# Performance work log

Hardware: AMD Instinct MI355X
Metric: run time of the kernel (lower is better)

The kernel has to match this reference:

```python
import jax, jax.numpy as jnp
import numpy as np

B, N, F_IN, D = 32768, 4, 512, 64  # N fixed to 4 by the max_pool(4,1)+reshape


def setup_inputs() -> dict:
    key = jax.random.key(0)
    k1, k2, k3, k4 = jax.random.split(key, 4)
    scale = 1.0 / np.sqrt(F_IN)
    return {
        "drug": jax.random.normal(k1, (B, N, F_IN), dtype=jnp.float32),
        "Wk": jax.random.normal(k2, (F_IN, D), dtype=jnp.float32) * scale,
        "Wq": jax.random.normal(k3, (F_IN, D), dtype=jnp.float32) * scale,
        "Wv": jax.random.normal(k4, (F_IN, D), dtype=jnp.float32) * scale,
    }


def reference(drug, Wk, Wq, Wv):
    # projections: torch nn.Linear(bias=False) -> x @ W  (W stored as [in, out] here)
    k = jnp.einsum("bnf,fd->bnd", drug, Wk)
    q = jnp.einsum("bnf,fd->bnd", drug, Wq)
    v = jnp.einsum("bnf,fd->bnd", drug, Wv)
    # score = bmm(K, Q^T); NOTE: no 1/sqrt(d) scaling, matching the source
    score = jnp.einsum("bnd,bmd->bnm", k, q)  # [B, N, N]
    attn = jax.nn.softmax(score, axis=2)
    out = jnp.einsum("bnm,bmd->bnd", attn, v)  # [B, N, D]
    # max_pool2d kernel (4,1), stride (4,1) over N=4 -> max over axis 1, then reshape [B, D]
    return jnp.max(out, axis=1)
```

## Files before the change

kernel.cpp:

```cpp
#include <hip/hip_runtime.h>
#include <hip/hip_fp16.h>

#define BTOT   32768
#define FIN    512
#define KSTEPS 16
#define NTILES 12
#define WH_ELEMS (KSTEPS * NTILES * 64 * 8)
#define CHUNK_HALVES (NTILES * 64 * 8)
#define KQ_HALVES (KSTEPS * 8 * 512)
#define KQ_BYTES  (KQ_HALVES * 2)
#define WAVES  8
#define ROWTILES 4
#define ROWS_PER_BLOCK (WAVES * 16 * ROWTILES)
#define NBLOCKS (BTOT * 4 / ROWS_PER_BLOCK)

using half8   = __attribute__((ext_vector_type(8))) _Float16;
using floatx4 = __attribute__((ext_vector_type(4))) float;

#define GLOAD_LDS16(gp, lp)                                                  \
    __builtin_amdgcn_global_load_lds(                                        \
        (const __attribute__((address_space(1))) void*)(gp),                 \
        (__attribute__((address_space(3))) void*)(lp), 16, 0, 0)

__global__ void convert_w_kernel(const float* __restrict__ Wk,
                                 const float* __restrict__ Wq,
                                 const float* __restrict__ Wv,
                                 _Float16* __restrict__ Wh) {
    int idx = blockIdx.x * blockDim.x + threadIdx.x;
    if (idx >= WH_ELEMS) return;
    int j    = idx & 7;
    int lane = (idx >> 3) & 63;
    int t    = (idx >> 9) % NTILES;
    int kk   = idx / CHUNK_HALVES;
    int k = kk * 32 + (lane >> 4) * 8 + j;
    int n = t * 16 + (lane & 15);
    const float* src = (n < 64) ? Wk : (n < 128) ? Wq : Wv;
    _Float16 val = (_Float16)src[k * 64 + (n & 63)];
    size_t dst = (t < 8)
        ? ((size_t)(kk * 8 + t) * 512 + lane * 8 + j)
        : (size_t)KQ_HALVES + ((size_t)(kk * 4 + (t - 8)) * 512 + lane * 8 + j);
    Wh[dst] = val;
}

__global__ __launch_bounds__(512, 2) void attn_fused_kernel(
        const float* __restrict__ drug,
        const _Float16* __restrict__ Wh,
        float* __restrict__ out)
{
    extern __shared__ __align__(16) char lds[];

    const int tid  = threadIdx.x;
    const int wave = tid >> 6;
    const int lane = tid & 63;
    const int quad = lane >> 4;
    const int l15  = lane & 15;

    {
        const char* gk = (const char*)Wh;
#pragma unroll
        for (int i = 0; i < 16; ++i) {
            const int off = i * 8192 + wave * 1024;
            GLOAD_LDS16(gk + off + lane * 16, lds + off);
        }
    }

    const half8* vf = (const half8*)(Wh + KQ_HALVES) + lane;

    const int rowbase = blockIdx.x * ROWS_PER_BLOCK + wave * 16 + l15;
    const float* arow = drug + (size_t)rowbase * FIN + quad * 8;
    float4 a0 = ((const float4*)arow)[0];
    float4 a1 = ((const float4*)arow)[1];
    half8 v0 = vf[0], v1 = vf[64], v2 = vf[128], v3 = vf[192];

    asm volatile("s_waitcnt vmcnt(0)" ::: "memory");
    __builtin_amdgcn_s_barrier();

    const int bbase = blockIdx.x * (ROWS_PER_BLOCK / 4) + wave * 4 + quad;

#pragma unroll 1
    for (int rt = 0; rt < ROWTILES; ++rt) {
        floatx4 acc[NTILES];
#pragma unroll
        for (int t = 0; t < NTILES; ++t) acc[t] = (floatx4){0.f, 0.f, 0.f, 0.f};

        const float* pfrow = (rt < ROWTILES - 1) ? arow + 128 * FIN : arow;

#pragma unroll 1
        for (int k = 0; k < KSTEPS; ++k) {
            float4 n0, n1;
            half8 w0, w1, w2, w3;
            {
                const float4* ap = (k < KSTEPS - 1)
                    ? (const float4*)(arow + (k + 1) * 32)
                    : (const float4*)pfrow;
                n0 = ap[0];
                n1 = ap[1];
                const half8* vp = (k < KSTEPS - 1) ? vf + (k + 1) * 256 : vf;
                w0 = vp[0]; w1 = vp[64]; w2 = vp[128]; w3 = vp[192];
            }

            half8 af;
            af[0] = (_Float16)a0.x; af[1] = (_Float16)a0.y;
            af[2] = (_Float16)a0.z; af[3] = (_Float16)a0.w;
            af[4] = (_Float16)a1.x; af[5] = (_Float16)a1.y;
            af[6] = (_Float16)a1.z; af[7] = (_Float16)a1.w;

            const _Float16* lh = (const _Float16*)(lds + k * 8192);
#pragma unroll
            for (int t = 0; t < 8; ++t) {
                half8 bf = *((const half8*)(lh + t * 512 + lane * 8));
                acc[t] = __builtin_amdgcn_mfma_f32_16x16x32_f16(af, bf, acc[t], 0, 0, 0);
            }
            acc[8]  = __builtin_amdgcn_mfma_f32_16x16x32_f16(af, v0, acc[8],  0, 0, 0);
            acc[9]  = __builtin_amdgcn_mfma_f32_16x16x32_f16(af, v1, acc[9],  0, 0, 0);
            acc[10] = __builtin_amdgcn_mfma_f32_16x16x32_f16(af, v2, acc[10], 0, 0, 0);
            acc[11] = __builtin_amdgcn_mfma_f32_16x16x32_f16(af, v3, acc[11], 0, 0, 0);

            a0 = n0; a1 = n1;
            v0 = w0; v1 = w1; v2 = w2; v3 = w3;
        }
        arow += 128 * FIN;

        float p[4][4];
#pragma unroll
        for (int n = 0; n < 4; ++n)
#pragma unroll
            for (int m = 0; m < 4; ++m) {
                float s = 0.f;
#pragma unroll
                for (int t = 0; t < 4; ++t) s += acc[t][n] * acc[4 + t][m];
                p[n][m] = s;
            }

#pragma unroll
        for (int mask = 1; mask < 16; mask <<= 1) {
#pragma unroll
            for (int n = 0; n < 4; ++n)
#pragma unroll
                for (int m = 0; m < 4; ++m)
                    p[n][m] += __shfl_xor(p[n][m], mask, 64);
        }

        float res[4] = {-INFINITY, -INFINITY, -INFINITY, -INFINITY};
#pragma unroll
        for (int n = 0; n < 4; ++n) {
            float mx = fmaxf(fmaxf(p[n][0], p[n][1]), fmaxf(p[n][2], p[n][3]));
            float e0 = __expf(p[n][0] - mx);
            float e1 = __expf(p[n][1] - mx);
            float e2 = __expf(p[n][2] - mx);
            float e3 = __expf(p[n][3] - mx);
            float inv = 1.f / (e0 + e1 + e2 + e3);
#pragma unroll
            for (int t = 0; t < 4; ++t) {
                float o = (e0 * acc[8 + t][0] + e1 * acc[8 + t][1] +
                           e2 * acc[8 + t][2] + e3 * acc[8 + t][3]) * inv;
                res[t] = fmaxf(res[t], o);
            }
        }

        const int b = bbase + rt * 32;
#pragma unroll
        for (int t = 0; t < 4; ++t)
            out[b * 64 + t * 16 + l15] = res[t];
    }
}

extern "C" void kernel_launch(void* const* d_in, const int* in_sizes, int n_in,
                              void* d_out, int out_size, void* d_ws, size_t ws_size,
                              hipStream_t stream) {
    const float* drug = (const float*)d_in[0];
    const float* Wk   = (const float*)d_in[1];
    const float* Wq   = (const float*)d_in[2];
    const float* Wv   = (const float*)d_in[3];
    float* out = (float*)d_out;
    _Float16* Wh = (_Float16*)d_ws;

    static bool attr_set = false;
    if (!attr_set) {
        hipFuncSetAttribute((const void*)attn_fused_kernel,
                            hipFuncAttributeMaxDynamicSharedMemorySize, KQ_BYTES);
        attr_set = true;
    }

    convert_w_kernel<<<(WH_ELEMS + 255) / 256, 256, 0, stream>>>(Wk, Wq, Wv, Wh);
    attn_fused_kernel<<<NBLOCKS, 512, KQ_BYTES, stream>>>(drug, Wh, out);
}
```

Measured before the change: 371.7 us.

## Process two row tiles per k-step and stage half of Wv in LDS

The main loop now keeps two 16-row A fragments and two accumulator sets, so each K/Q/V B-fragment loaded from LDS or registers feeds two MFMAs. Two of the four V tiles now sit in LDS (160KB total) instead of being reloaded from global memory every k-step. The row loop becomes two passes of paired tiles, with a shared epilogue helper. The aim is to halve LDS and global weight traffic per MFMA. The cost is doubled accumulator and prefetch register pressure under launch_bounds(512,2), which risks spilling, and a larger LDS footprint that limits blocks per CU.

```diff
diff --git a/kernel.cpp b/kernel.cpp
--- a/kernel.cpp
+++ b/kernel.cpp
@@ -6,12 +6,11 @@
 #define KSTEPS 16
 #define NTILES 12
 #define WH_ELEMS (KSTEPS * NTILES * 64 * 8)
-#define CHUNK_HALVES (NTILES * 64 * 8)
-#define KQ_HALVES (KSTEPS * 8 * 512)
-#define KQ_BYTES  (KQ_HALVES * 2)
+#define KQ_HALVES  65536
+#define V23_BASE   81920
+#define LDS_BYTES  163840
 #define WAVES  8
-#define ROWTILES 4
-#define ROWS_PER_BLOCK (WAVES * 16 * ROWTILES)
+#define ROWS_PER_BLOCK 512
 #define NBLOCKS (BTOT * 4 / ROWS_PER_BLOCK)
 
 using half8   = __attribute__((ext_vector_type(8))) _Float16;
@@ -31,15 +30,61 @@
     int j    = idx & 7;
     int lane = (idx >> 3) & 63;
     int t    = (idx >> 9) % NTILES;
-    int kk   = idx / CHUNK_HALVES;
+    int kk   = idx / (NTILES * 64 * 8);
     int k = kk * 32 + (lane >> 4) * 8 + j;
     int n = t * 16 + (lane & 15);
     const float* src = (n < 64) ? Wk : (n < 128) ? Wq : Wv;
     _Float16 val = (_Float16)src[k * 64 + (n & 63)];
-    size_t dst = (t < 8)
-        ? ((size_t)(kk * 8 + t) * 512 + lane * 8 + j)
-        : (size_t)KQ_HALVES + ((size_t)(kk * 4 + (t - 8)) * 512 + lane * 8 + j);
+    size_t dst;
+    if (t < 8)
+        dst = (size_t)(kk * 8 + t) * 512 + lane * 8 + j;
+    else if (t < 10)
+        dst = (size_t)KQ_HALVES + (size_t)(kk * 2 + (t - 8)) * 512 + lane * 8 + j;
+    else
+        dst = (size_t)V23_BASE + (size_t)(kk * 2 + (t - 10)) * 512 + lane * 8 + j;
     Wh[dst] = val;
+}
+
+__device__ __forceinline__ void attn_epilogue(const floatx4 (&acc)[NTILES],
+                                              float* __restrict__ out,
+                                              int b, int l15) {
+    float p[4][4];
+#pragma unroll
+    for (int n = 0; n < 4; ++n)
+#pragma unroll
+        for (int m = 0; m < 4; ++m) {
+            float s = 0.f;
+#pragma unroll
+            for (int t = 0; t < 4; ++t) s += acc[t][n] * acc[4 + t][m];
+            p[n][m] = s;
+        }
+#pragma unroll
+    for (int mask = 1; mask < 16; mask <<= 1) {
+#pragma unroll
+        for (int n = 0; n < 4; ++n)
+#pragma unroll
+            for (int m = 0; m < 4; ++m)
+                p[n][m] += __shfl_xor(p[n][m], mask, 64);
+    }
+    float res[4] = {-INFINITY, -INFINITY, -INFINITY, -INFINITY};
+#pragma unroll
+    for (int n = 0; n < 4; ++n) {
+        float mx = fmaxf(fmaxf(p[n][0], p[n][1]), fmaxf(p[n][2], p[n][3]));
+        float e0 = __expf(p[n][0] - mx);
+        float e1 = __expf(p[n][1] - mx);
+        float e2 = __expf(p[n][2] - mx);
+        float e3 = __expf(p[n][3] - mx);
+        float inv = 1.f / (e0 + e1 + e2 + e3);
+#pragma unroll
+        for (int t = 0; t < 4; ++t) {
+            float o = (e0 * acc[8 + t][0] + e1 * acc[8 + t][1] +
+                       e2 * acc[8 + t][2] + e3 * acc[8 + t][3]) * inv;
+            res[t] = fmaxf(res[t], o);
+        }
+    }
+#pragma unroll
+    for (int t = 0; t < 4; ++t)
+        out[b * 64 + t * 16 + l15] = res[t];
 }
 
 __global__ __launch_bounds__(512, 2) void attn_fused_kernel(
@@ -56,112 +101,90 @@
     const int l15  = lane & 15;
 
     {
-        const char* gk = (const char*)Wh;
-#pragma unroll
-        for (int i = 0; i < 16; ++i) {
+        const char* gW = (const char*)Wh;
+#pragma unroll
+        for (int i = 0; i < 20; ++i) {
             const int off = i * 8192 + wave * 1024;
-            GLOAD_LDS16(gk + off + lane * 16, lds + off);
-        }
-    }
-
-    const half8* vf = (const half8*)(Wh + KQ_HALVES) + lane;
-
-    const int rowbase = blockIdx.x * ROWS_PER_BLOCK + wave * 16 + l15;
-    const float* arow = drug + (size_t)rowbase * FIN + quad * 8;
-    float4 a0 = ((const float4*)arow)[0];
-    float4 a1 = ((const float4*)arow)[1];
-    half8 v0 = vf[0], v1 = vf[64], v2 = vf[128], v3 = vf[192];
+            GLOAD_LDS16(gW + off + lane * 16, lds + off);
+        }
+    }
+
+    const half8* vg = (const half8*)(Wh + V23_BASE) + lane;
+
+    const size_t row0 = (size_t)blockIdx.x * ROWS_PER_BLOCK + wave * 16 + l15;
+    const float* abase = drug + row0 * FIN + quad * 8;
+
+    float4 a00 = ((const float4*)abase)[0];
+    float4 a01 = ((const float4*)abase)[1];
+    const float* abase1 = abase + 128 * FIN;
+    float4 a10 = ((const float4*)abase1)[0];
+    float4 a11 = ((const float4*)abase1)[1];
+    half8 w0 = vg[0], w1 = vg[64];
 
     asm volatile("s_waitcnt vmcnt(0)" ::: "memory");
     __builtin_amdgcn_s_barrier();
 
-    const int bbase = blockIdx.x * (ROWS_PER_BLOCK / 4) + wave * 4 + quad;
-
 #pragma unroll 1
-    for (int rt = 0; rt < ROWTILES; ++rt) {
-        floatx4 acc[NTILES];
-#pragma unroll
-        for (int t = 0; t < NTILES; ++t) acc[t] = (floatx4){0.f, 0.f, 0.f, 0.f};
-
-        const float* pfrow = (rt < ROWTILES - 1) ? arow + 128 * FIN : arow;
+    for (int pass = 0; pass < 2; ++pass) {
+        const float* ar0 = abase + (size_t)pass * 256 * FIN;
+
+        floatx4 acc0[NTILES], acc1[NTILES];
+#pragma unroll
+        for (int t = 0; t < NTILES; ++t) {
+            acc0[t] = (floatx4){0.f, 0.f, 0.f, 0.f};
+            acc1[t] = (floatx4){0.f, 0.f, 0.f, 0.f};
+        }
 
 #pragma unroll 1
         for (int k = 0; k < KSTEPS; ++k) {
-            float4 n0, n1;
-            half8 w0, w1, w2, w3;
-            {
-                const float4* ap = (k < KSTEPS - 1)
-                    ? (const float4*)(arow + (k + 1) * 32)
-                    : (const float4*)pfrow;
-                n0 = ap[0];
-                n1 = ap[1];
-                const half8* vp = (k < KSTEPS - 1) ? vf + (k + 1) * 256 : vf;
-                w0 = vp[0]; w1 = vp[64]; w2 = vp[128]; w3 = vp[192];
+            const int kn = (k < KSTEPS - 1) ? (k + 1) : 0;
+            const float* pr0 = (k < KSTEPS - 1)
+                ? (ar0 + (k + 1) * 32)
+                : (ar0 + ((pass == 0) ? 256 * FIN : 0));
+            const float* pr1 = pr0 + 128 * FIN;
+            float4 n00 = ((const float4*)pr0)[0];
+            float4 n01 = ((const float4*)pr0)[1];
+            float4 n10 = ((const float4*)pr1)[0];
+            float4 n11 = ((const float4*)pr1)[1];
+            const half8* vp = vg + kn * 128;
+            half8 nw0 = vp[0], nw1 = vp[64];
+
+            half8 af0, af1;
+            af0[0] = (_Float16)a00.x; af0[1] = (_Float16)a00.y;
+            af0[2] = (_Float16)a00.z; af0[3] = (_Float16)a00.w;
+            af0[4] = (_Float16)a01.x; af0[5] = (_Float16)a01.y;
+            af0[6] = (_Float16)a01.z; af0[7] = (_Float16)a01.w;
+            af1[0] = (_Float16)a10.x; af1[1] = (_Float16)a10.y;
+            af1[2] = (_Float16)a10.z; af1[3] = (_Float16)a10.w;
+            af1[4] = (_Float16)a11.x; af1[5] = (_Float16)a11.y;
+            af1[6] = (_Float16)a11.z; af1[7] = (_Float16)a11.w;
+
+            const _Float16* lk = (const _Float16*)(lds + k * 8192);
+#pragma unroll
+            for (int t = 0; t < 8; ++t) {
+                half8 bf = *((const half8*)(lk + t * 512 + lane * 8));
+                acc0[t] = __builtin_amdgcn_mfma_f32_16x16x32_f16(af0, bf, acc0[t], 0, 0, 0);
+                acc1[t] = __builtin_amdgcn_mfma_f32_16x16x32_f16(af1, bf, acc1[t], 0, 0, 0);
             }
-
-            half8 af;
-            af[0] = (_Float16)a0.x; af[1] = (_Float16)a0.y;
-            af[2] = (_Float16)a0.z; af[3] = (_Float16)a0.w;
-            af[4] = (_Float16)a1.x; af[5] = (_Float16)a1.y;
-            af[6] = (_Float16)a1.z; af[7] = (_Float16)a1.w;
-
-            const _Float16* lh = (const _Float16*)(lds + k * 8192);
-#pragma unroll
-            for (int t = 0; t < 8; ++t) {
-                half8 bf = *((const half8*)(lh + t * 512 + lane * 8));
-                acc[t] = __builtin_amdgcn_mfma_f32_16x16x32_f16(af, bf, acc[t], 0, 0, 0);
+            const _Float16* lv = (const _Float16*)(lds + 131072 + k * 2048);
+#pragma unroll
+            for (int tv = 0; tv < 2; ++tv) {
+                half8 bv = *((const half8*)(lv + tv * 512 + lane * 8));
+                acc0[8 + tv] = __builtin_amdgcn_mfma_f32_16x16x32_f16(af0, bv, acc0[8 + tv], 0, 0, 0);
+                acc1[8 + tv] = __builtin_amdgcn_mfma_f32_16x16x32_f16(af1, bv, acc1[8 + tv], 0, 0, 0);
             }
-            acc[8]  = __builtin_amdgcn_mfma_f32_16x16x32_f16(af, v0, acc[8],  0, 0, 0);
-            acc[9]  = __builtin_amdgcn_mfma_f32_16x16x32_f16(af, v1, acc[9],  0, 0, 0);
-            acc[10] = __builtin_amdgcn_mfma_f32_16x16x32_f16(af, v2, acc[10], 0, 0, 0);
-            acc[11] = __builtin_amdgcn_mfma_f32_16x16x32_f16(af, v3, acc[11], 0, 0, 0);
-
-            a0 = n0; a1 = n1;
-            v0 = w0; v1 = w1; v2 = w2; v3 = w3;
-        }
-        arow += 128 * FIN;
-
-        float p[4][4];
-#pragma unroll
-        for (int n = 0; n < 4; ++n)
-#pragma unroll
-            for (int m = 0; m < 4; ++m) {
-                float s = 0.f;
-#pragma unroll
-                for (int t = 0; t < 4; ++t) s += acc[t][n] * acc[4 + t][m];
-                p[n][m] = s;
-            }
-
-#pragma unroll
-        for (int mask = 1; mask < 16; mask <<= 1) {
-#pragma unroll
-            for (int n = 0; n < 4; ++n)
-#pragma unroll
-                for (int m = 0; m < 4; ++m)
-                    p[n][m] += __shfl_xor(p[n][m], mask, 64);
-        }
-
-        float res[4] = {-INFINITY, -INFINITY, -INFINITY, -INFINITY};
-#pragma unroll
-        for (int n = 0; n < 4; ++n) {
-            float mx = fmaxf(fmaxf(p[n][0], p[n][1]), fmaxf(p[n][2], p[n][3]));
-            float e0 = __expf(p[n][0] - mx);
-            float e1 = __expf(p[n][1] - mx);
-            float e2 = __expf(p[n][2] - mx);
-            float e3 = __expf(p[n][3] - mx);
-            float inv = 1.f / (e0 + e1 + e2 + e3);
-#pragma unroll
-            for (int t = 0; t < 4; ++t) {
-                float o = (e0 * acc[8 + t][0] + e1 * acc[8 + t][1] +
-                           e2 * acc[8 + t][2] + e3 * acc[8 + t][3]) * inv;
-                res[t] = fmaxf(res[t], o);
-            }
-        }
-
-        const int b = bbase + rt * 32;
-#pragma unroll
-        for (int t = 0; t < 4; ++t)
-            out[b * 64 + t * 16 + l15] = res[t];
+            acc0[10] = __builtin_amdgcn_mfma_f32_16x16x32_f16(af0, w0, acc0[10], 0, 0, 0);
+            acc1[10] = __builtin_amdgcn_mfma_f32_16x16x32_f16(af1, w0, acc1[10], 0, 0, 0);
+            acc0[11] = __builtin_amdgcn_mfma_f32_16x16x32_f16(af0, w1, acc0[11], 0, 0, 0);
+            acc1[11] = __builtin_amdgcn_mfma_f32_16x16x32_f16(af1, w1, acc1[11], 0, 0, 0);
+
+            a00 = n00; a01 = n01; a10 = n10; a11 = n11;
+            w0 = nw0; w1 = nw1;
+        }
+
+        const int b0 = blockIdx.x * 128 + pass * 64 + wave * 4 + quad;
+        attn_epilogue(acc0, out, b0, l15);
+        attn_epilogue(acc1, out, b0 + 32, l15);
     }
 }
 
@@ -178,10 +201,10 @@
     static bool attr_set = false;
     if (!attr_set) {
         hipFuncSetAttribute((const void*)attn_fused_kernel,
-                            hipFuncAttributeMaxDynamicSharedMemorySize, KQ_BYTES);
+                            hipFuncAttributeMaxDynamicSharedMemorySize, LDS_BYTES);
         attr_set = true;
     }
 
     convert_w_kernel<<<(WH_ELEMS + 255) / 256, 256, 0, stream>>>(Wk, Wq, Wv, Wh);
-    attn_fused_kernel<<<NBLOCKS, 512, KQ_BYTES, stream>>>(drug, Wh, out);
-}
+    attn_fused_kernel<<<NBLOCKS, 512, LDS_BYTES, stream>>>(drug, Wh, out);
+}
```

Result: no change. 368.6 us (-0.8%).
